# Optimization experiments

Hardware: AMD Instinct MI355X
Metric: run time of the kernel (lower is better)

## Reference

```python
import jax, jax.numpy as jnp
import numpy as np

B, T, D, NH, L = 8192, 100, 44, 64, 8  # batch, seq/ode steps, obs_dim, rnn hidden, latent


def setup_inputs() -> dict:
    key = jax.random.key(0)
    ks = jax.random.split(key, 12)
    s = 0.1
    return {
        "x": jax.random.normal(ks[0], (B, T, D), jnp.float32),
        "mask": jax.random.randint(ks[1], (B, T, D), 0, 2).astype(jnp.float32),
        "epsilon": jax.random.normal(ks[2], (B, L), jnp.float32),
        "Wi2h": jax.random.normal(ks[3], (D + NH, NH), jnp.float32) * s,
        "bi2h": jnp.zeros((NH,), jnp.float32),
        "Wh2o": jax.random.normal(ks[4], (NH, 2 * L), jnp.float32) * s,
        "bh2o": jnp.zeros((2 * L,), jnp.float32),
        "Wf1": jax.random.normal(ks[5], (L, NH), jnp.float32) * s,
        "bf1": jnp.zeros((NH,), jnp.float32),
        "Wf2": jax.random.normal(ks[6], (NH, NH), jnp.float32) * s,
        "bf2": jnp.zeros((NH,), jnp.float32),
        "Wf3": jax.random.normal(ks[7], (NH, L), jnp.float32) * s,
        "bf3": jnp.zeros((L,), jnp.float32),
        "Wd1": jax.random.normal(ks[8], (L, NH), jnp.float32) * s,
        "bd1": jnp.zeros((NH,), jnp.float32),
        "Wd2": jax.random.normal(ks[9], (NH, D), jnp.float32) * s,
        "bd2": jnp.zeros((D,), jnp.float32),
    }


def reference(x, mask, epsilon, Wi2h, bi2h, Wh2o, bh2o,
              Wf1, bf1, Wf2, bf2, Wf3, bf3, Wd1, bd1, Wd2, bd2):
    masked_x = x * mask  # [B,T,D]

    # --- reverse-time recognition RNN (scan over time, reversed) ---
    def rnn_step(h, obs):
        h = jnp.tanh(jnp.concatenate([obs, h], axis=1) @ Wi2h + bi2h)
        return h, None

    xs_rev = jnp.transpose(masked_x[:, ::-1, :], (1, 0, 2))  # [T,B,D]
    h0 = jnp.zeros((x.shape[0], Wi2h.shape[1]), x.dtype)
    h_final, _ = jax.lax.scan(rnn_step, h0, xs_rev)
    out = h_final @ Wh2o + bh2o  # [B,2L]
    qz0_mean, qz0_logvar = out[:, :L], out[:, L:]

    # reparameterized latent sample
    z0 = epsilon * jnp.exp(0.5 * qz0_logvar) + qz0_mean  # [B,L]

    # --- latent ODE dynamics, fixed-step RK4 over ts = linspace(0,1,100) ---
    def f(z):
        h1 = jax.nn.elu(z @ Wf1 + bf1)
        h2 = jax.nn.elu(h1 @ Wf2 + bf2)
        return h2 @ Wf3 + bf3

    dt = jnp.asarray(1.0 / (T - 1), x.dtype)

    def rk4_step(z, _):
        k1 = f(z)
        k2 = f(z + 0.5 * dt * k1)
        k3 = f(z + 0.5 * dt * k2)
        k4 = f(z + dt * k3)
        zn = z + (dt / 6.0) * (k1 + 2.0 * k2 + 2.0 * k3 + k4)
        return zn, zn

    _, zs = jax.lax.scan(rk4_step, z0, None, length=T - 1)  # [T-1,B,L]
    pred_z = jnp.transpose(jnp.concatenate([z0[None], zs], axis=0), (1, 0, 2))  # [B,T,L]

    # --- decoder ---
    pred_x = jax.nn.relu(pred_z @ Wd1 + bd1) @ Wd2 + bd2  # [B,T,D]

    # fill observed entries back in
    updated_x = jnp.where(masked_x != 0, masked_x, pred_x)

    # --- loss ---
    noise_logvar = 2.0 * jnp.log(jnp.asarray(0.3, x.dtype))
    log2pi = jnp.log(jnp.asarray(2.0 * np.pi, x.dtype))
    logpx = (-0.5 * (log2pi + noise_logvar +
                     (x - updated_x) ** 2 / jnp.exp(noise_logvar))).sum((-1, -2))  # [B]
    kl = (-0.5 * qz0_logvar + (jnp.exp(qz0_logvar) + qz0_mean ** 2) / 2.0 - 0.5).sum(-1)  # [B]
    loss = jnp.mean(-logpx + kl)
    return loss
```

## Files before the change

kernel.cpp:

```cpp
#include <hip/hip_runtime.h>
#include <stdint.h>


constexpr int B_ = 8192, T_ = 100, D_ = 44, NH_ = 64, L_ = 8;

typedef __bf16 bf16x8 __attribute__((ext_vector_type(8)));
typedef float f32x4 __attribute__((ext_vector_type(4)));
typedef uint32_t u32x4 __attribute__((ext_vector_type(4)));
typedef uint32_t u32x2 __attribute__((ext_vector_type(2)));

__device__ __forceinline__ float fexp2(float x) { return __builtin_amdgcn_exp2f(x); }
__device__ __forceinline__ float frcp(float x) { return __builtin_amdgcn_rcpf(x); }
__device__ __forceinline__ float fexp(float x) { return fexp2(x * 1.44269504088896341f); }
__device__ __forceinline__ float tanh_f(float x) {
  float e = fexp2(x * 2.88539008177792681f);
  return 1.0f - 2.0f * frcp(e + 1.0f);
}
__device__ __forceinline__ float elu_f(float x) { return x > 0.0f ? x : (fexp(x) - 1.0f); }
__device__ __forceinline__ uint32_t f2bs(float x) {
  return (uint32_t)__builtin_bit_cast(unsigned short, (__bf16)x);
}
__device__ __forceinline__ uint32_t pk(float lo, float hi) { return f2bs(lo) | (f2bs(hi) << 16); }
__device__ __forceinline__ uint32_t sh(uint32_t v, int s) { return (uint32_t)__shfl((int)v, s, 64); }
__device__ __forceinline__ f32x4 mfma16(bf16x8 a, bf16x8 b, f32x4 c) {
  return __builtin_amdgcn_mfma_f32_16x16x32_bf16(a, b, c, 0, 0, 0);
}
__device__ __forceinline__ bf16x8 pack8(float a, float b, float c, float d,
                                        float e, float f, float g, float h) {
  u32x4 u = {pk(a, b), pk(c, d), pk(e, f), pk(g, h)};
  return __builtin_bit_cast(bf16x8, u);
}
__device__ __forceinline__ float f4get(const float4& f, int i) {
  return i == 0 ? f.x : (i == 1 ? f.y : (i == 2 ? f.z : f.w));
}

__device__ __forceinline__ void repack_lds(uint32_t* tb, int c, int q,
                                           const f32x4* e, bf16x8* bh) {
#pragma unroll
  for (int tau = 0; tau < 4; ++tau) {
    u32x2 w = {pk(e[tau][0], e[tau][1]), pk(e[tau][2], e[tau][3])};
    *(u32x2*)(tb + 36 * c + 8 * tau + 2 * q) = w;
  }
#pragma unroll
  for (int ks = 0; ks < 2; ++ks) {
    u32x4 r = *(const u32x4*)(tb + 36 * c + 16 * ks + 4 * q);
    bh[ks] = __builtin_bit_cast(bf16x8, r);
  }
}

__device__ __forceinline__ bf16x8 build_bz(f32x4 z, int c, int q) {
  uint32_t p01 = pk(z[0], z[1]), p23 = pk(z[2], z[3]);
  u32x4 u = {sh(p01, c), sh(p23, c), sh(p01, c + 16), sh(p23, c + 16)};
  if (q == 1) u[0] = 0x3f80u;
  return __builtin_bit_cast(bf16x8, u);
}

__global__ __launch_bounds__(64) void fused_kernel(
    const float* __restrict__ x, const float* __restrict__ mask,
    const float* __restrict__ eps,
    const float* __restrict__ Wi2h, const float* __restrict__ bi2h,
    const float* __restrict__ Wh2o, const float* __restrict__ bh2o,
    const float* __restrict__ Wf1, const float* __restrict__ bf1,
    const float* __restrict__ Wf2, const float* __restrict__ bf2,
    const float* __restrict__ Wf3, const float* __restrict__ bf3,
    const float* __restrict__ Wd1, const float* __restrict__ bd1,
    const float* __restrict__ Wd2, const float* __restrict__ bd2,
    float* __restrict__ part) {
  const int lane = threadIdx.x;
  const int c = lane & 15, q = lane >> 4;
  const int r0 = blockIdx.x * 16;

  __shared__ uint32_t tbufA[576];
  __shared__ uint32_t tbufB[576];

  bf16x8 Ai[4][4];
#pragma unroll
  for (int tau = 0; tau < 4; ++tau)
#pragma unroll
    for (int ks = 0; ks < 4; ++ks) {
      bf16x8 f;
      const int m = 16 * tau + c;
#pragma unroll
      for (int i = 0; i < 8; ++i) {
        const int k = 32 * ks + 8 * q + i;
        float v = 0.0f;
        if (k < 64) v = Wi2h[(44 + k) * 64 + m];
        else if (k < 108) v = Wi2h[(k - 64) * 64 + m];
        else if (k == 108) v = bi2h[m];
        f[i] = (__bf16)v;
      }
      Ai[tau][ks] = f;
    }
  bf16x8 Ah2o[2];
#pragma unroll
  for (int ks = 0; ks < 2; ++ks) {
    bf16x8 f;
#pragma unroll
    for (int i = 0; i < 8; ++i) f[i] = (__bf16)Wh2o[(32 * ks + 8 * q + i) * 16 + c];
    Ah2o[ks] = f;
  }
  f32x4 bo;
#pragma unroll
  for (int r = 0; r < 4; ++r) bo[r] = bh2o[4 * q + r];

  const float* xrowbase = x + (size_t)(r0 + c) * T_ * D_;
  const float* mrowbase = mask + (size_t)(r0 + c) * T_ * D_;

  auto load_obs = [&](int t, float4& a0, float4& a1, float4& b0, float4& b1,
                      float4& ma0, float4& ma1, float4& mb0, float4& mb1) {
    const float4* xr = (const float4*)(xrowbase + (size_t)t * D_);
    const float4* mr = (const float4*)(mrowbase + (size_t)t * D_);
    a0 = xr[2 * q]; a1 = xr[2 * q + 1]; ma0 = mr[2 * q]; ma1 = mr[2 * q + 1];
    float4 zz = {0.f, 0.f, 0.f, 0.f};
    b0 = zz; b1 = zz; mb0 = zz; mb1 = zz;
    if (q == 0) { b0 = xr[8]; b1 = xr[9]; mb0 = mr[8]; mb1 = mr[9]; }
    else if (q == 1) { b0 = xr[10]; mb0 = mr[10]; }
  };

  f32x4 hc[4] = {};
  float4 a0, a1, b0, b1, ma0, ma1, mb0, mb1;
  load_obs(T_ - 1, a0, a1, b0, b1, ma0, ma1, mb0, mb1);

#pragma unroll 1
  for (int s = 0; s < T_; ++s) {
    const int t = T_ - 1 - s;
    float4 ca0 = a0, ca1 = a1, cb0 = b0, cb1 = b1;
    float4 cm0 = ma0, cm1 = ma1, cn0 = mb0, cn1 = mb1;
    if (t > 0) load_obs(t - 1, a0, a1, b0, b1, ma0, ma1, mb0, mb1);

    bf16x8 bh[2];
    repack_lds(tbufA, c, q, hc, bh);
    bf16x8 o2 = pack8(ca0.x * cm0.x, ca0.y * cm0.y, ca0.z * cm0.z, ca0.w * cm0.w,
                      ca1.x * cm1.x, ca1.y * cm1.y, ca1.z * cm1.z, ca1.w * cm1.w);
    const float e44 = (q == 1) ? 1.0f : cb1.x * cn1.x;
    bf16x8 o3 = pack8(cb0.x * cn0.x, cb0.y * cn0.y, cb0.z * cn0.z, cb0.w * cn0.w,
                      e44, cb1.y * cn1.y, cb1.z * cn1.z, cb1.w * cn1.w);
#pragma unroll
    for (int tau = 0; tau < 4; ++tau) {
      f32x4 zero = {0.f, 0.f, 0.f, 0.f};
      f32x4 acc = mfma16(Ai[tau][0], bh[0], zero);
      acc = mfma16(Ai[tau][1], bh[1], acc);
      acc = mfma16(Ai[tau][2], o2, acc);
      acc = mfma16(Ai[tau][3], o3, acc);
#pragma unroll
      for (int r = 0; r < 4; ++r) hc[tau][r] = tanh_f(acc[r]);
    }
  }

  bf16x8 bhF[2];
  repack_lds(tbufA, c, q, hc, bhF);
  f32x4 o = mfma16(Ah2o[1], bhF[1], mfma16(Ah2o[0], bhF[0], bo));

  float lv[4];
#pragma unroll
  for (int r = 0; r < 4; ++r)
    lv[r] = __int_as_float(__shfl(__float_as_int(o[r]), lane + 32, 64));

  float klt = 0.0f;
  f32x4 z = {};
  if (q < 2) {
    const float4 ev = *(const float4*)(eps + (size_t)(r0 + c) * 8 + 4 * q);
#pragma unroll
    for (int r = 0; r < 4; ++r) {
      const float m = o[r];
      z[r] = f4get(ev, r) * fexp(0.5f * lv[r]) + m;
      klt += -0.5f * lv[r] + (fexp(lv[r]) + m * m) * 0.5f - 0.5f;
    }
  }
  klt += __shfl_xor(klt, 1);  klt += __shfl_xor(klt, 2);
  klt += __shfl_xor(klt, 4);  klt += __shfl_xor(klt, 8);
  klt += __shfl_xor(klt, 16); klt += __shfl_xor(klt, 32);

  __builtin_amdgcn_sched_barrier(0);

  bf16x8 A1[4], A2[4][2], A3[2], Ad1[4], Ad2[3][2];
#pragma unroll
  for (int tau = 0; tau < 4; ++tau) {
    bf16x8 f1, fd;
#pragma unroll
    for (int i = 0; i < 8; ++i) {
      const int k = 8 * q + i;
      f1[i] = (__bf16)(k < 8 ? Wf1[k * 64 + 16 * tau + c] : (k == 8 ? bf1[16 * tau + c] : 0.0f));
      fd[i] = (__bf16)(k < 8 ? Wd1[k * 64 + 16 * tau + c] : (k == 8 ? bd1[16 * tau + c] : 0.0f));
    }
    A1[tau] = f1; Ad1[tau] = fd;
#pragma unroll
    for (int ks = 0; ks < 2; ++ks) {
      bf16x8 g;
#pragma unroll
      for (int i = 0; i < 8; ++i) g[i] = (__bf16)Wf2[(32 * ks + 8 * q + i) * 64 + 16 * tau + c];
      A2[tau][ks] = g;
    }
  }
#pragma unroll
  for (int ks = 0; ks < 2; ++ks) {
    bf16x8 f;
#pragma unroll
    for (int i = 0; i < 8; ++i)
      f[i] = (__bf16)((c < 8) ? Wf3[(32 * ks + 8 * q + i) * 8 + c] : 0.0f);
    A3[ks] = f;
  }
#pragma unroll
  for (int tau = 0; tau < 3; ++tau)
#pragma unroll
    for (int ks = 0; ks < 2; ++ks) {
      bf16x8 f;
      const int m = 16 * tau + c;
#pragma unroll
      for (int i = 0; i < 8; ++i)
        f[i] = (__bf16)((m < 44) ? Wd2[(32 * ks + 8 * q + i) * 44 + m] : 0.0f);
      Ad2[tau][ks] = f;
    }
  f32x4 b2_[4], b3_, bd2_[3];
#pragma unroll
  for (int tau = 0; tau < 4; ++tau)
#pragma unroll
    for (int r = 0; r < 4; ++r) b2_[tau][r] = bf2[16 * tau + 4 * q + r];
#pragma unroll
  for (int r = 0; r < 4; ++r) b3_[r] = (q < 2) ? bf3[4 * q + r] : 0.0f;
#pragma unroll
  for (int tau = 0; tau < 3; ++tau)
#pragma unroll
    for (int r = 0; r < 4; ++r) {
      const int d = 16 * tau + 4 * q + r;
      bd2_[tau][r] = (d < 44) ? bd2[d] : 0.0f;
    }

  auto feval = [&](bf16x8 bz) -> f32x4 {
    f32x4 h[4];
#pragma unroll
    for (int tau = 0; tau < 4; ++tau) {
      f32x4 zero = {0.f, 0.f, 0.f, 0.f};
      h[tau] = mfma16(A1[tau], bz, zero);
#pragma unroll
      for (int r = 0; r < 4; ++r) h[tau][r] = elu_f(h[tau][r]);
    }
    bf16x8 bh[2];
    repack_lds(tbufA, c, q, h, bh);
    f32x4 g[4];
#pragma unroll
    for (int tau = 0; tau < 4; ++tau) {
      g[tau] = mfma16(A2[tau][1], bh[1], mfma16(A2[tau][0], bh[0], b2_[tau]));
#pragma unroll
      for (int r = 0; r < 4; ++r) g[tau][r] = elu_f(g[tau][r]);
    }
    bf16x8 bg[2];
    repack_lds(tbufA, c, q, g, bg);
    return mfma16(A3[1], bg[1], mfma16(A3[0], bg[0], b3_));
  };

  auto load_xm = [&](int t, float4* xv, float4* mv) {
#pragma unroll
    for (int tau = 0; tau < 3; ++tau) {
      const int d0 = 16 * tau + 4 * q;
      if (d0 < 44) {
        const size_t off = (size_t)(r0 + c) * T_ * D_ + (size_t)t * D_ + d0;
        xv[tau] = *(const float4*)(x + off);
        mv[tau] = *(const float4*)(mask + off);
      }
    }
  };

  const float dt = 1.0f / (float)(T_ - 1);
  const float hdt = 0.5f * dt;
  float qacc = 0.0f;

  float4 xc[3], mc[3], xn[3], mn[3];
  load_xm(0, xc, mc);

#pragma unroll 1
  for (int t = 0; t < T_; ++t) {
    if (t < T_ - 1) load_xm(t + 1, xn, mn);

    bf16x8 bz = build_bz(z, c, q);

    f32x4 hd[4];
#pragma unroll
    for (int tau = 0; tau < 4; ++tau) {
      f32x4 zero = {0.f, 0.f, 0.f, 0.f};
      hd[tau] = mfma16(Ad1[tau], bz, zero);
#pragma unroll
      for (int r = 0; r < 4; ++r) hd[tau][r] = fmaxf(hd[tau][r], 0.0f);
    }
    bf16x8 bhd[2];
    repack_lds(tbufB, c, q, hd, bhd);
#pragma unroll
    for (int tau = 0; tau < 3; ++tau) {
      f32x4 p = mfma16(Ad2[tau][1], bhd[1], mfma16(Ad2[tau][0], bhd[0], bd2_[tau]));
      if (16 * tau + 4 * q < 44) {
#pragma unroll
        for (int r = 0; r < 4; ++r) {
          const float xa = f4get(xc[tau], r), ma = f4get(mc[tau], r);
          const float mx = xa * ma;
          const float upd = (mx != 0.0f) ? mx : p[r];
          const float df = xa - upd;
          qacc += df * df;
        }
      }
    }

    if (t < T_ - 1) {
      f32x4 k1 = feval(bz);
      f32x4 zt;
#pragma unroll
      for (int r = 0; r < 4; ++r) zt[r] = z[r] + hdt * k1[r];
      f32x4 k2 = feval(build_bz(zt, c, q));
#pragma unroll
      for (int r = 0; r < 4; ++r) zt[r] = z[r] + hdt * k2[r];
      f32x4 k3 = feval(build_bz(zt, c, q));
#pragma unroll
      for (int r = 0; r < 4; ++r) zt[r] = z[r] + dt * k3[r];
      f32x4 k4 = feval(build_bz(zt, c, q));
#pragma unroll
      for (int r = 0; r < 4; ++r)
        z[r] += (dt / 6.0f) * (k1[r] + 2.0f * (k2[r] + k3[r]) + k4[r]);
#pragma unroll
      for (int tau = 0; tau < 3; ++tau) { xc[tau] = xn[tau]; mc[tau] = mn[tau]; }
    }
  }

  float tot = qacc * (0.5f / 0.09f);
  tot += __shfl_xor(tot, 1);  tot += __shfl_xor(tot, 2);
  tot += __shfl_xor(tot, 4);  tot += __shfl_xor(tot, 8);
  tot += __shfl_xor(tot, 16); tot += __shfl_xor(tot, 32);
  if (lane == 0) part[blockIdx.x] = tot + klt;
}

__global__ __launch_bounds__(512) void reduce_kernel(const float* __restrict__ part,
                                                     float* __restrict__ out) {
  __shared__ float s[8];
  const int tid = threadIdx.x;
  float v = part[tid];
  v += __shfl_xor(v, 1);  v += __shfl_xor(v, 2);
  v += __shfl_xor(v, 4);  v += __shfl_xor(v, 8);
  v += __shfl_xor(v, 16); v += __shfl_xor(v, 32);
  if ((tid & 63) == 0) s[tid >> 6] = v;
  __syncthreads();
  if (tid == 0) {
    float acc = 0.0f;
#pragma unroll
    for (int i = 0; i < 8; ++i) acc += s[i];
    const float c0 = 0.28503427112126353f;
    out[0] = acc * (1.0f / (float)B_) - (float)(T_ * D_) * c0;
  }
}

extern "C" void kernel_launch(void* const* d_in, const int* in_sizes, int n_in,
                              void* d_out, int out_size, void* d_ws, size_t ws_size,
                              hipStream_t stream) {
  const float* x    = (const float*)d_in[0];
  const float* mask = (const float*)d_in[1];
  const float* eps  = (const float*)d_in[2];
  const float* Wi2h = (const float*)d_in[3];
  const float* bi2h = (const float*)d_in[4];
  const float* Wh2o = (const float*)d_in[5];
  const float* bh2o = (const float*)d_in[6];
  const float* Wf1  = (const float*)d_in[7];
  const float* bf1  = (const float*)d_in[8];
  const float* Wf2  = (const float*)d_in[9];
  const float* bf2  = (const float*)d_in[10];
  const float* Wf3  = (const float*)d_in[11];
  const float* bf3  = (const float*)d_in[12];
  const float* Wd1  = (const float*)d_in[13];
  const float* bd1  = (const float*)d_in[14];
  const float* Wd2  = (const float*)d_in[15];
  const float* bd2  = (const float*)d_in[16];

  float* loss = (float*)d_out;
  float* part = (float*)d_ws;

  fused_kernel<<<dim3(B_ / 16), dim3(64), 0, stream>>>(
      x, mask, eps, Wi2h, bi2h, Wh2o, bh2o, Wf1, bf1, Wf2, bf2, Wf3, bf3,
      Wd1, bd1, Wd2, bd2, part);
  reduce_kernel<<<dim3(1), dim3(512), 0, stream>>>(part, loss);
}
```

Baseline: 826.9 us.

## Split hidden-unit tiles across four waves per block with LDS exchange

Each 16-row batch tile now runs on a 256-thread block in which every wave owns one 16-wide slice of the 64 hidden units. The four tau tiles that one wave used to compute serially are spread across waves, and hidden states are exchanged through double-buffered LDS with a workgroup barrier at each layer. The goal is to cut the serial MFMA and transcendental chain per timestep and to hold fewer weight registers per wave. The cost is several barriers per RNN and RK4 step, plus more waves per block, which could shift occupancy.

Result: faster. 757.2 us (-8.4%).

```diff
diff --git a/kernel.cpp b/kernel.cpp
--- a/kernel.cpp
+++ b/kernel.cpp
@@ -34,16 +34,20 @@
   return i == 0 ? f.x : (i == 1 ? f.y : (i == 2 ? f.z : f.w));
 }
 
-__device__ __forceinline__ void repack_lds(uint32_t* tb, int c, int q,
-                                           const f32x4* e, bf16x8* bh) {
-#pragma unroll
-  for (int tau = 0; tau < 4; ++tau) {
-    u32x2 w = {pk(e[tau][0], e[tau][1]), pk(e[tau][2], e[tau][3])};
-    *(u32x2*)(tb + 36 * c + 8 * tau + 2 * q) = w;
-  }
-#pragma unroll
-  for (int ks = 0; ks < 2; ++ks) {
-    u32x4 r = *(const u32x4*)(tb + 36 * c + 16 * ks + 4 * q);
+__device__ __forceinline__ void xbar() {
+  asm volatile("s_waitcnt lgkmcnt(0)" ::: "memory");
+  __builtin_amdgcn_s_barrier();
+  asm volatile("" ::: "memory");
+}
+
+__device__ __forceinline__ void ex_write(uint32_t* ex, int c, int q, int w, f32x4 e) {
+  u32x2 v = {pk(e[0], e[1]), pk(e[2], e[3])};
+  *(u32x2*)(ex + 36 * c + 8 * w + 2 * q) = v;
+}
+__device__ __forceinline__ void ex_read(const uint32_t* ex, int c, int q, bf16x8* bh) {
+#pragma unroll
+  for (int ks = 0; ks < 2; ++ks) {
+    u32x4 r = *(const u32x4*)(ex + 36 * c + 16 * ks + 4 * q);
     bh[ks] = __builtin_bit_cast(bf16x8, r);
   }
 }
@@ -55,7 +59,7 @@
   return __builtin_bit_cast(bf16x8, u);
 }
 
-__global__ __launch_bounds__(64) void fused_kernel(
+__global__ __launch_bounds__(256) void fused_kernel(
     const float* __restrict__ x, const float* __restrict__ mask,
     const float* __restrict__ eps,
     const float* __restrict__ Wi2h, const float* __restrict__ bi2h,
@@ -66,31 +70,33 @@
     const float* __restrict__ Wd1, const float* __restrict__ bd1,
     const float* __restrict__ Wd2, const float* __restrict__ bd2,
     float* __restrict__ part) {
-  const int lane = threadIdx.x;
+  const int tid = threadIdx.x;
+  const int w = tid >> 6;
+  const int lane = tid & 63;
   const int c = lane & 15, q = lane >> 4;
   const int r0 = blockIdx.x * 16;
 
-  __shared__ uint32_t tbufA[576];
-  __shared__ uint32_t tbufB[576];
-
-  bf16x8 Ai[4][4];
-#pragma unroll
-  for (int tau = 0; tau < 4; ++tau)
-#pragma unroll
-    for (int ks = 0; ks < 4; ++ks) {
-      bf16x8 f;
-      const int m = 16 * tau + c;
-#pragma unroll
-      for (int i = 0; i < 8; ++i) {
-        const int k = 32 * ks + 8 * q + i;
-        float v = 0.0f;
-        if (k < 64) v = Wi2h[(44 + k) * 64 + m];
-        else if (k < 108) v = Wi2h[(k - 64) * 64 + m];
-        else if (k == 108) v = bi2h[m];
-        f[i] = (__bf16)v;
-      }
-      Ai[tau][ks] = f;
-    }
+  __shared__ __align__(16) uint32_t exA[576];
+  __shared__ __align__(16) uint32_t exB[576];
+  __shared__ __align__(16) uint32_t exC[576];
+  __shared__ float redbuf[4];
+
+  bf16x8 Ai[4];
+#pragma unroll
+  for (int ks = 0; ks < 4; ++ks) {
+    bf16x8 f;
+    const int m = 16 * w + c;
+#pragma unroll
+    for (int i = 0; i < 8; ++i) {
+      const int k = 32 * ks + 8 * q + i;
+      float v = 0.0f;
+      if (k < 64) v = Wi2h[(44 + k) * 64 + m];
+      else if (k < 108) v = Wi2h[(k - 64) * 64 + m];
+      else if (k == 108) v = bi2h[m];
+      f[i] = (__bf16)v;
+    }
+    Ai[ks] = f;
+  }
   bf16x8 Ah2o[2];
 #pragma unroll
   for (int ks = 0; ks < 2; ++ks) {
@@ -117,38 +123,43 @@
     else if (q == 1) { b0 = xr[10]; mb0 = mr[10]; }
   };
 
-  f32x4 hc[4] = {};
+  f32x4 hc = {0.f, 0.f, 0.f, 0.f};
   float4 a0, a1, b0, b1, ma0, ma1, mb0, mb1;
   load_obs(T_ - 1, a0, a1, b0, b1, ma0, ma1, mb0, mb1);
 
 #pragma unroll 1
   for (int s = 0; s < T_; ++s) {
+    uint32_t* ex = (s & 1) ? exB : exA;
+    ex_write(ex, c, q, w, hc);
+
     const int t = T_ - 1 - s;
     float4 ca0 = a0, ca1 = a1, cb0 = b0, cb1 = b1;
     float4 cm0 = ma0, cm1 = ma1, cn0 = mb0, cn1 = mb1;
     if (t > 0) load_obs(t - 1, a0, a1, b0, b1, ma0, ma1, mb0, mb1);
 
-    bf16x8 bh[2];
-    repack_lds(tbufA, c, q, hc, bh);
     bf16x8 o2 = pack8(ca0.x * cm0.x, ca0.y * cm0.y, ca0.z * cm0.z, ca0.w * cm0.w,
                       ca1.x * cm1.x, ca1.y * cm1.y, ca1.z * cm1.z, ca1.w * cm1.w);
     const float e44 = (q == 1) ? 1.0f : cb1.x * cn1.x;
     bf16x8 o3 = pack8(cb0.x * cn0.x, cb0.y * cn0.y, cb0.z * cn0.z, cb0.w * cn0.w,
                       e44, cb1.y * cn1.y, cb1.z * cn1.z, cb1.w * cn1.w);
-#pragma unroll
-    for (int tau = 0; tau < 4; ++tau) {
-      f32x4 zero = {0.f, 0.f, 0.f, 0.f};
-      f32x4 acc = mfma16(Ai[tau][0], bh[0], zero);
-      acc = mfma16(Ai[tau][1], bh[1], acc);
-      acc = mfma16(Ai[tau][2], o2, acc);
-      acc = mfma16(Ai[tau][3], o3, acc);
-#pragma unroll
-      for (int r = 0; r < 4; ++r) hc[tau][r] = tanh_f(acc[r]);
-    }
-  }
-
+
+    xbar();
+    bf16x8 bh[2];
+    ex_read(ex, c, q, bh);
+
+    f32x4 zero = {0.f, 0.f, 0.f, 0.f};
+    f32x4 acc = mfma16(Ai[0], bh[0], zero);
+    acc = mfma16(Ai[1], bh[1], acc);
+    acc = mfma16(Ai[2], o2, acc);
+    acc = mfma16(Ai[3], o3, acc);
+#pragma unroll
+    for (int r = 0; r < 4; ++r) hc[r] = tanh_f(acc[r]);
+  }
+
+  ex_write(exA, c, q, w, hc);
+  xbar();
   bf16x8 bhF[2];
-  repack_lds(tbufA, c, q, hc, bhF);
+  ex_read(exA, c, q, bhF);
   f32x4 o = mfma16(Ah2o[1], bhF[1], mfma16(Ah2o[0], bhF[0], bo));
 
   float lv[4];
@@ -173,24 +184,23 @@
 
   __builtin_amdgcn_sched_barrier(0);
 
-  bf16x8 A1[4], A2[4][2], A3[2], Ad1[4], Ad2[3][2];
-#pragma unroll
-  for (int tau = 0; tau < 4; ++tau) {
+  bf16x8 A1, A2[2], A3[2], Ad1, Ad2[2];
+  {
     bf16x8 f1, fd;
 #pragma unroll
     for (int i = 0; i < 8; ++i) {
       const int k = 8 * q + i;
-      f1[i] = (__bf16)(k < 8 ? Wf1[k * 64 + 16 * tau + c] : (k == 8 ? bf1[16 * tau + c] : 0.0f));
-      fd[i] = (__bf16)(k < 8 ? Wd1[k * 64 + 16 * tau + c] : (k == 8 ? bd1[16 * tau + c] : 0.0f));
-    }
-    A1[tau] = f1; Ad1[tau] = fd;
-#pragma unroll
-    for (int ks = 0; ks < 2; ++ks) {
-      bf16x8 g;
-#pragma unroll
-      for (int i = 0; i < 8; ++i) g[i] = (__bf16)Wf2[(32 * ks + 8 * q + i) * 64 + 16 * tau + c];
-      A2[tau][ks] = g;
-    }
+      f1[i] = (__bf16)(k < 8 ? Wf1[k * 64 + 16 * w + c] : (k == 8 ? bf1[16 * w + c] : 0.0f));
+      fd[i] = (__bf16)(k < 8 ? Wd1[k * 64 + 16 * w + c] : (k == 8 ? bd1[16 * w + c] : 0.0f));
+    }
+    A1 = f1; Ad1 = fd;
+  }
+#pragma unroll
+  for (int ks = 0; ks < 2; ++ks) {
+    bf16x8 g;
+#pragma unroll
+    for (int i = 0; i < 8; ++i) g[i] = (__bf16)Wf2[(32 * ks + 8 * q + i) * 64 + 16 * w + c];
+    A2[ks] = g;
   }
 #pragma unroll
   for (int ks = 0; ks < 2; ++ks) {
@@ -201,63 +211,50 @@
     A3[ks] = f;
   }
 #pragma unroll
-  for (int tau = 0; tau < 3; ++tau)
-#pragma unroll
-    for (int ks = 0; ks < 2; ++ks) {
-      bf16x8 f;
-      const int m = 16 * tau + c;
-#pragma unroll
-      for (int i = 0; i < 8; ++i)
-        f[i] = (__bf16)((m < 44) ? Wd2[(32 * ks + 8 * q + i) * 44 + m] : 0.0f);
-      Ad2[tau][ks] = f;
-    }
-  f32x4 b2_[4], b3_, bd2_[3];
-#pragma unroll
-  for (int tau = 0; tau < 4; ++tau)
-#pragma unroll
-    for (int r = 0; r < 4; ++r) b2_[tau][r] = bf2[16 * tau + 4 * q + r];
+  for (int ks = 0; ks < 2; ++ks) {
+    bf16x8 f;
+    const int m = 16 * w + c;
+#pragma unroll
+    for (int i = 0; i < 8; ++i)
+      f[i] = (__bf16)((m < 44) ? Wd2[(32 * ks + 8 * q + i) * 44 + m] : 0.0f);
+    Ad2[ks] = f;
+  }
+  f32x4 b2_, b3_, bd2_;
+#pragma unroll
+  for (int r = 0; r < 4; ++r) b2_[r] = bf2[16 * w + 4 * q + r];
 #pragma unroll
   for (int r = 0; r < 4; ++r) b3_[r] = (q < 2) ? bf3[4 * q + r] : 0.0f;
 #pragma unroll
-  for (int tau = 0; tau < 3; ++tau)
-#pragma unroll
-    for (int r = 0; r < 4; ++r) {
-      const int d = 16 * tau + 4 * q + r;
-      bd2_[tau][r] = (d < 44) ? bd2[d] : 0.0f;
-    }
+  for (int r = 0; r < 4; ++r) {
+    const int d = 16 * w + 4 * q + r;
+    bd2_[r] = (d < 44) ? bd2[d] : 0.0f;
+  }
 
   auto feval = [&](bf16x8 bz) -> f32x4 {
-    f32x4 h[4];
-#pragma unroll
-    for (int tau = 0; tau < 4; ++tau) {
-      f32x4 zero = {0.f, 0.f, 0.f, 0.f};
-      h[tau] = mfma16(A1[tau], bz, zero);
-#pragma unroll
-      for (int r = 0; r < 4; ++r) h[tau][r] = elu_f(h[tau][r]);
-    }
+    f32x4 zero = {0.f, 0.f, 0.f, 0.f};
+    f32x4 h = mfma16(A1, bz, zero);
+#pragma unroll
+    for (int r = 0; r < 4; ++r) h[r] = elu_f(h[r]);
+    ex_write(exA, c, q, w, h);
+    xbar();
     bf16x8 bh[2];
-    repack_lds(tbufA, c, q, h, bh);
-    f32x4 g[4];
-#pragma unroll
-    for (int tau = 0; tau < 4; ++tau) {
-      g[tau] = mfma16(A2[tau][1], bh[1], mfma16(A2[tau][0], bh[0], b2_[tau]));
-#pragma unroll
-      for (int r = 0; r < 4; ++r) g[tau][r] = elu_f(g[tau][r]);
-    }
+    ex_read(exA, c, q, bh);
+    f32x4 g = mfma16(A2[1], bh[1], mfma16(A2[0], bh[0], b2_));
+#pragma unroll
+    for (int r = 0; r < 4; ++r) g[r] = elu_f(g[r]);
+    ex_write(exB, c, q, w, g);
+    xbar();
     bf16x8 bg[2];
-    repack_lds(tbufA, c, q, g, bg);
+    ex_read(exB, c, q, bg);
     return mfma16(A3[1], bg[1], mfma16(A3[0], bg[0], b3_));
   };
 
-  auto load_xm = [&](int t, float4* xv, float4* mv) {
-#pragma unroll
-    for (int tau = 0; tau < 3; ++tau) {
-      const int d0 = 16 * tau + 4 * q;
-      if (d0 < 44) {
-        const size_t off = (size_t)(r0 + c) * T_ * D_ + (size_t)t * D_ + d0;
-        xv[tau] = *(const float4*)(x + off);
-        mv[tau] = *(const float4*)(mask + off);
-      }
+  auto load_xm = [&](int t, float4& xv, float4& mv) {
+    const int d0 = 16 * w + 4 * q;
+    if (w < 3 && d0 < 44) {
+      const size_t off = (size_t)(r0 + c) * T_ * D_ + (size_t)t * D_ + d0;
+      xv = *(const float4*)(x + off);
+      mv = *(const float4*)(mask + off);
     }
   };
 
@@ -265,7 +262,7 @@
   const float hdt = 0.5f * dt;
   float qacc = 0.0f;
 
-  float4 xc[3], mc[3], xn[3], mn[3];
+  float4 xc = {0.f, 0.f, 0.f, 0.f}, mc = xc, xn = xc, mn = xc;
   load_xm(0, xc, mc);
 
 #pragma unroll 1
@@ -274,23 +271,20 @@
 
     bf16x8 bz = build_bz(z, c, q);
 
-    f32x4 hd[4];
-#pragma unroll
-    for (int tau = 0; tau < 4; ++tau) {
-      f32x4 zero = {0.f, 0.f, 0.f, 0.f};
-      hd[tau] = mfma16(Ad1[tau], bz, zero);
-#pragma unroll
-      for (int r = 0; r < 4; ++r) hd[tau][r] = fmaxf(hd[tau][r], 0.0f);
-    }
-    bf16x8 bhd[2];
-    repack_lds(tbufB, c, q, hd, bhd);
-#pragma unroll
-    for (int tau = 0; tau < 3; ++tau) {
-      f32x4 p = mfma16(Ad2[tau][1], bhd[1], mfma16(Ad2[tau][0], bhd[0], bd2_[tau]));
-      if (16 * tau + 4 * q < 44) {
+    f32x4 zero = {0.f, 0.f, 0.f, 0.f};
+    f32x4 hd = mfma16(Ad1, bz, zero);
+#pragma unroll
+    for (int r = 0; r < 4; ++r) hd[r] = fmaxf(hd[r], 0.0f);
+    ex_write(exC, c, q, w, hd);
+    xbar();
+    if (w < 3) {
+      bf16x8 bhd[2];
+      ex_read(exC, c, q, bhd);
+      f32x4 p = mfma16(Ad2[1], bhd[1], mfma16(Ad2[0], bhd[0], bd2_));
+      if (16 * w + 4 * q < 44) {
 #pragma unroll
         for (int r = 0; r < 4; ++r) {
-          const float xa = f4get(xc[tau], r), ma = f4get(mc[tau], r);
+          const float xa = f4get(xc, r), ma = f4get(mc, r);
           const float mx = xa * ma;
           const float upd = (mx != 0.0f) ? mx : p[r];
           const float df = xa - upd;
@@ -314,8 +308,7 @@
 #pragma unroll
       for (int r = 0; r < 4; ++r)
         z[r] += (dt / 6.0f) * (k1[r] + 2.0f * (k2[r] + k3[r]) + k4[r]);
-#pragma unroll
-      for (int tau = 0; tau < 3; ++tau) { xc[tau] = xn[tau]; mc[tau] = mn[tau]; }
+      xc = xn; mc = mn;
     }
   }
 
@@ -323,7 +316,10 @@
   tot += __shfl_xor(tot, 1);  tot += __shfl_xor(tot, 2);
   tot += __shfl_xor(tot, 4);  tot += __shfl_xor(tot, 8);
   tot += __shfl_xor(tot, 16); tot += __shfl_xor(tot, 32);
-  if (lane == 0) part[blockIdx.x] = tot + klt;
+  if (lane == 0) redbuf[w] = tot;
+  xbar();
+  if (tid == 0)
+    part[blockIdx.x] = redbuf[0] + redbuf[1] + redbuf[2] + redbuf[3] + klt;
 }
 
 __global__ __launch_bounds__(512) void reduce_kernel(const float* __restrict__ part,
@@ -369,7 +365,7 @@
   float* loss = (float*)d_out;
   float* part = (float*)d_ws;
 
-  fused_kernel<<<dim3(B_ / 16), dim3(64), 0, stream>>>(
+  fused_kernel<<<dim3(B_ / 16), dim3(256), 0, stream>>>(
       x, mask, eps, Wi2h, bi2h, Wh2o, bh2o, Wf1, bf1, Wf2, bf2, Wf3, bf3,
       Wd1, bd1, Wd2, bd2, part);
   reduce_kernel<<<dim3(1), dim3(512), 0, stream>>>(part, loss);
```

## Switch to 16x16x16 MFMA so accumulator layout feeds next B operand without LDS

Applied to the files above, without the earlier changes.

Replaces the 16x16x32 bf16 MFMA with the 16x16x16 variant, whose C/D fragment layout (4 rows per lane group) matches the B operand layout. This lets each layer's output be packed directly in registers as the next layer's input, removing the LDS write/read repacks and the shuffles in build_bz. It doubles the MFMA instruction count for the same K and splits the RNN accumulation into two independent chains to shorten dependency latency.

New measurement: 698.0 us. 15.6% less time.

```diff
diff --git a/kernel.cpp b/kernel.cpp
--- a/kernel.cpp
+++ b/kernel.cpp
@@ -4,10 +4,26 @@
 
 constexpr int B_ = 8192, T_ = 100, D_ = 44, NH_ = 64, L_ = 8;
 
-typedef __bf16 bf16x8 __attribute__((ext_vector_type(8)));
 typedef float f32x4 __attribute__((ext_vector_type(4)));
-typedef uint32_t u32x4 __attribute__((ext_vector_type(4)));
 typedef uint32_t u32x2 __attribute__((ext_vector_type(2)));
+
+#if __has_builtin(__builtin_amdgcn_mfma_f32_16x16x16bf16_1k)
+typedef short frag16 __attribute__((ext_vector_type(4)));
+#define MFMA16(a, b, c) __builtin_amdgcn_mfma_f32_16x16x16bf16_1k(a, b, c, 0, 0, 0)
+#define USE_F16 0
+#elif __has_builtin(__builtin_amdgcn_mfma_f32_16x16x16_bf16_1k)
+typedef short frag16 __attribute__((ext_vector_type(4)));
+#define MFMA16(a, b, c) __builtin_amdgcn_mfma_f32_16x16x16_bf16_1k(a, b, c, 0, 0, 0)
+#define USE_F16 0
+#elif __has_builtin(__builtin_amdgcn_mfma_f32_16x16x16_bf16)
+typedef __bf16 frag16 __attribute__((ext_vector_type(4)));
+#define MFMA16(a, b, c) __builtin_amdgcn_mfma_f32_16x16x16_bf16(a, b, c, 0, 0, 0)
+#define USE_F16 0
+#else
+typedef _Float16 frag16 __attribute__((ext_vector_type(4)));
+#define MFMA16(a, b, c) __builtin_amdgcn_mfma_f32_16x16x16f16(a, b, c, 0, 0, 0)
+#define USE_F16 1
+#endif
 
 __device__ __forceinline__ float fexp2(float x) { return __builtin_amdgcn_exp2f(x); }
 __device__ __forceinline__ float frcp(float x) { return __builtin_amdgcn_rcpf(x); }
@@ -17,42 +33,25 @@
   return 1.0f - 2.0f * frcp(e + 1.0f);
 }
 __device__ __forceinline__ float elu_f(float x) { return x > 0.0f ? x : (fexp(x) - 1.0f); }
-__device__ __forceinline__ uint32_t f2bs(float x) {
-  return (uint32_t)__builtin_bit_cast(unsigned short, (__bf16)x);
-}
-__device__ __forceinline__ uint32_t pk(float lo, float hi) { return f2bs(lo) | (f2bs(hi) << 16); }
-__device__ __forceinline__ uint32_t sh(uint32_t v, int s) { return (uint32_t)__shfl((int)v, s, 64); }
-__device__ __forceinline__ f32x4 mfma16(bf16x8 a, bf16x8 b, f32x4 c) {
-  return __builtin_amdgcn_mfma_f32_16x16x32_bf16(a, b, c, 0, 0, 0);
-}
-__device__ __forceinline__ bf16x8 pack8(float a, float b, float c, float d,
-                                        float e, float f, float g, float h) {
-  u32x4 u = {pk(a, b), pk(c, d), pk(e, f), pk(g, h)};
-  return __builtin_bit_cast(bf16x8, u);
+
+__device__ __forceinline__ uint32_t EW(float v) {
+#if USE_F16
+  return (uint32_t)__builtin_bit_cast(unsigned short, (_Float16)v);
+#else
+  return (uint32_t)__builtin_bit_cast(unsigned short, (__bf16)v);
+#endif
+}
+__device__ __forceinline__ uint32_t PK2(float lo, float hi) { return EW(lo) | (EW(hi) << 16); }
+__device__ __forceinline__ frag16 fr4(float a, float b, float c, float d) {
+  u32x2 u = {PK2(a, b), PK2(c, d)};
+  return __builtin_bit_cast(frag16, u);
+}
+__device__ __forceinline__ frag16 frpk(f32x4 v) {
+  u32x2 u = {PK2(v[0], v[1]), PK2(v[2], v[3])};
+  return __builtin_bit_cast(frag16, u);
 }
 __device__ __forceinline__ float f4get(const float4& f, int i) {
   return i == 0 ? f.x : (i == 1 ? f.y : (i == 2 ? f.z : f.w));
-}
-
-__device__ __forceinline__ void repack_lds(uint32_t* tb, int c, int q,
-                                           const f32x4* e, bf16x8* bh) {
-#pragma unroll
-  for (int tau = 0; tau < 4; ++tau) {
-    u32x2 w = {pk(e[tau][0], e[tau][1]), pk(e[tau][2], e[tau][3])};
-    *(u32x2*)(tb + 36 * c + 8 * tau + 2 * q) = w;
-  }
-#pragma unroll
-  for (int ks = 0; ks < 2; ++ks) {
-    u32x4 r = *(const u32x4*)(tb + 36 * c + 16 * ks + 4 * q);
-    bh[ks] = __builtin_bit_cast(bf16x8, r);
-  }
-}
-
-__device__ __forceinline__ bf16x8 build_bz(f32x4 z, int c, int q) {
-  uint32_t p01 = pk(z[0], z[1]), p23 = pk(z[2], z[3]);
-  u32x4 u = {sh(p01, c), sh(p23, c), sh(p01, c + 16), sh(p23, c + 16)};
-  if (q == 1) u[0] = 0x3f80u;
-  return __builtin_bit_cast(bf16x8, u);
 }
 
 __global__ __launch_bounds__(64) void fused_kernel(
@@ -69,35 +68,34 @@
   const int lane = threadIdx.x;
   const int c = lane & 15, q = lane >> 4;
   const int r0 = blockIdx.x * 16;
-
-  __shared__ uint32_t tbufA[576];
-  __shared__ uint32_t tbufB[576];
-
-  bf16x8 Ai[4][4];
+  const f32x4 fzero = {0.f, 0.f, 0.f, 0.f};
+  const frag16 fgbias = fr4(1.0f, 0.f, 0.f, 0.f);
+
+  frag16 Ai[4][7];
 #pragma unroll
   for (int tau = 0; tau < 4; ++tau)
 #pragma unroll
-    for (int ks = 0; ks < 4; ++ks) {
-      bf16x8 f;
+    for (int kc = 0; kc < 7; ++kc) {
       const int m = 16 * tau + c;
-#pragma unroll
-      for (int i = 0; i < 8; ++i) {
-        const int k = 32 * ks + 8 * q + i;
+      float wv[4];
+#pragma unroll
+      for (int i = 0; i < 4; ++i) {
+        const int k = 16 * kc + 4 * q + i;
         float v = 0.0f;
         if (k < 64) v = Wi2h[(44 + k) * 64 + m];
         else if (k < 108) v = Wi2h[(k - 64) * 64 + m];
         else if (k == 108) v = bi2h[m];
-        f[i] = (__bf16)v;
+        wv[i] = v;
       }
-      Ai[tau][ks] = f;
-    }
-  bf16x8 Ah2o[2];
-#pragma unroll
-  for (int ks = 0; ks < 2; ++ks) {
-    bf16x8 f;
-#pragma unroll
-    for (int i = 0; i < 8; ++i) f[i] = (__bf16)Wh2o[(32 * ks + 8 * q + i) * 16 + c];
-    Ah2o[ks] = f;
+      Ai[tau][kc] = fr4(wv[0], wv[1], wv[2], wv[3]);
+    }
+  frag16 Ah2o[4];
+#pragma unroll
+  for (int kc = 0; kc < 4; ++kc) {
+    float wv[4];
+#pragma unroll
+    for (int i = 0; i < 4; ++i) wv[i] = Wh2o[(16 * kc + 4 * q + i) * 16 + c];
+    Ah2o[kc] = fr4(wv[0], wv[1], wv[2], wv[3]);
   }
   f32x4 bo;
 #pragma unroll
@@ -106,50 +104,70 @@
   const float* xrowbase = x + (size_t)(r0 + c) * T_ * D_;
   const float* mrowbase = mask + (size_t)(r0 + c) * T_ * D_;
 
-  auto load_obs = [&](int t, float4& a0, float4& a1, float4& b0, float4& b1,
-                      float4& ma0, float4& ma1, float4& mb0, float4& mb1) {
-    const float4* xr = (const float4*)(xrowbase + (size_t)t * D_);
-    const float4* mr = (const float4*)(mrowbase + (size_t)t * D_);
-    a0 = xr[2 * q]; a1 = xr[2 * q + 1]; ma0 = mr[2 * q]; ma1 = mr[2 * q + 1];
+  auto load_obs = [&](int t, float4* xv, float4* mv) {
+    const float* xp = xrowbase + (size_t)t * D_;
+    const float* mp = mrowbase + (size_t)t * D_;
+    xv[0] = *(const float4*)(xp + 4 * q);
+    mv[0] = *(const float4*)(mp + 4 * q);
+    xv[1] = *(const float4*)(xp + 16 + 4 * q);
+    mv[1] = *(const float4*)(mp + 16 + 4 * q);
     float4 zz = {0.f, 0.f, 0.f, 0.f};
-    b0 = zz; b1 = zz; mb0 = zz; mb1 = zz;
-    if (q == 0) { b0 = xr[8]; b1 = xr[9]; mb0 = mr[8]; mb1 = mr[9]; }
-    else if (q == 1) { b0 = xr[10]; mb0 = mr[10]; }
+    xv[2] = zz; mv[2] = zz;
+    if (q < 3) {
+      xv[2] = *(const float4*)(xp + 32 + 4 * q);
+      mv[2] = *(const float4*)(mp + 32 + 4 * q);
+    }
   };
 
   f32x4 hc[4] = {};
-  float4 a0, a1, b0, b1, ma0, ma1, mb0, mb1;
-  load_obs(T_ - 1, a0, a1, b0, b1, ma0, ma1, mb0, mb1);
+  float4 xo[3], mo[3];
+  load_obs(T_ - 1, xo, mo);
 
 #pragma unroll 1
   for (int s = 0; s < T_; ++s) {
     const int t = T_ - 1 - s;
-    float4 ca0 = a0, ca1 = a1, cb0 = b0, cb1 = b1;
-    float4 cm0 = ma0, cm1 = ma1, cn0 = mb0, cn1 = mb1;
-    if (t > 0) load_obs(t - 1, a0, a1, b0, b1, ma0, ma1, mb0, mb1);
-
-    bf16x8 bh[2];
-    repack_lds(tbufA, c, q, hc, bh);
-    bf16x8 o2 = pack8(ca0.x * cm0.x, ca0.y * cm0.y, ca0.z * cm0.z, ca0.w * cm0.w,
-                      ca1.x * cm1.x, ca1.y * cm1.y, ca1.z * cm1.z, ca1.w * cm1.w);
-    const float e44 = (q == 1) ? 1.0f : cb1.x * cn1.x;
-    bf16x8 o3 = pack8(cb0.x * cn0.x, cb0.y * cn0.y, cb0.z * cn0.z, cb0.w * cn0.w,
-                      e44, cb1.y * cn1.y, cb1.z * cn1.z, cb1.w * cn1.w);
+    float4 cx[3], cm[3];
+#pragma unroll
+    for (int j = 0; j < 3; ++j) { cx[j] = xo[j]; cm[j] = mo[j]; }
+    if (t > 0) load_obs(t - 1, xo, mo);
+
+    frag16 ob[3];
+#pragma unroll
+    for (int j = 0; j < 2; ++j) {
+      u32x2 u = {PK2(cx[j].x * cm[j].x, cx[j].y * cm[j].y),
+                 PK2(cx[j].z * cm[j].z, cx[j].w * cm[j].w)};
+      ob[j] = __builtin_bit_cast(frag16, u);
+    }
+    {
+      u32x2 u = {PK2(cx[2].x * cm[2].x, cx[2].y * cm[2].y),
+                 PK2(cx[2].z * cm[2].z, cx[2].w * cm[2].w)};
+      ob[2] = (q < 3) ? __builtin_bit_cast(frag16, u) : fgbias;
+    }
+
+    frag16 bh[4];
+#pragma unroll
+    for (int tau = 0; tau < 4; ++tau) bh[tau] = frpk(hc[tau]);
+
 #pragma unroll
     for (int tau = 0; tau < 4; ++tau) {
-      f32x4 zero = {0.f, 0.f, 0.f, 0.f};
-      f32x4 acc = mfma16(Ai[tau][0], bh[0], zero);
-      acc = mfma16(Ai[tau][1], bh[1], acc);
-      acc = mfma16(Ai[tau][2], o2, acc);
-      acc = mfma16(Ai[tau][3], o3, acc);
-#pragma unroll
-      for (int r = 0; r < 4; ++r) hc[tau][r] = tanh_f(acc[r]);
-    }
-  }
-
-  bf16x8 bhF[2];
-  repack_lds(tbufA, c, q, hc, bhF);
-  f32x4 o = mfma16(Ah2o[1], bhF[1], mfma16(Ah2o[0], bhF[0], bo));
+      f32x4 aA = MFMA16(Ai[tau][0], bh[0], fzero);
+      aA = MFMA16(Ai[tau][1], bh[1], aA);
+      aA = MFMA16(Ai[tau][2], bh[2], aA);
+      aA = MFMA16(Ai[tau][3], bh[3], aA);
+      f32x4 aB = MFMA16(Ai[tau][4], ob[0], fzero);
+      aB = MFMA16(Ai[tau][5], ob[1], aB);
+      aB = MFMA16(Ai[tau][6], ob[2], aB);
+#pragma unroll
+      for (int r = 0; r < 4; ++r) hc[tau][r] = tanh_f(aA[r] + aB[r]);
+    }
+  }
+
+  frag16 bhF[4];
+#pragma unroll
+  for (int tau = 0; tau < 4; ++tau) bhF[tau] = frpk(hc[tau]);
+  f32x4 o = bo;
+#pragma unroll
+  for (int kc = 0; kc < 4; ++kc) o = MFMA16(Ah2o[kc], bhF[kc], o);
 
   float lv[4];
 #pragma unroll
@@ -173,43 +191,46 @@
 
   __builtin_amdgcn_sched_barrier(0);
 
-  bf16x8 A1[4], A2[4][2], A3[2], Ad1[4], Ad2[3][2];
+  frag16 A1[4], A2[4][4], A3[4], Ad1[4], Ad2[3][4];
 #pragma unroll
   for (int tau = 0; tau < 4; ++tau) {
-    bf16x8 f1, fd;
-#pragma unroll
-    for (int i = 0; i < 8; ++i) {
-      const int k = 8 * q + i;
-      f1[i] = (__bf16)(k < 8 ? Wf1[k * 64 + 16 * tau + c] : (k == 8 ? bf1[16 * tau + c] : 0.0f));
-      fd[i] = (__bf16)(k < 8 ? Wd1[k * 64 + 16 * tau + c] : (k == 8 ? bd1[16 * tau + c] : 0.0f));
-    }
-    A1[tau] = f1; Ad1[tau] = fd;
-#pragma unroll
-    for (int ks = 0; ks < 2; ++ks) {
-      bf16x8 g;
-#pragma unroll
-      for (int i = 0; i < 8; ++i) g[i] = (__bf16)Wf2[(32 * ks + 8 * q + i) * 64 + 16 * tau + c];
-      A2[tau][ks] = g;
-    }
-  }
-#pragma unroll
-  for (int ks = 0; ks < 2; ++ks) {
-    bf16x8 f;
-#pragma unroll
-    for (int i = 0; i < 8; ++i)
-      f[i] = (__bf16)((c < 8) ? Wf3[(32 * ks + 8 * q + i) * 8 + c] : 0.0f);
-    A3[ks] = f;
+    float w1[4], wd[4];
+#pragma unroll
+    for (int i = 0; i < 4; ++i) {
+      const int k = 4 * q + i;
+      w1[i] = k < 8 ? Wf1[k * 64 + 16 * tau + c] : (k == 8 ? bf1[16 * tau + c] : 0.0f);
+      wd[i] = k < 8 ? Wd1[k * 64 + 16 * tau + c] : (k == 8 ? bd1[16 * tau + c] : 0.0f);
+    }
+    A1[tau] = fr4(w1[0], w1[1], w1[2], w1[3]);
+    Ad1[tau] = fr4(wd[0], wd[1], wd[2], wd[3]);
+  }
+#pragma unroll
+  for (int tau = 0; tau < 4; ++tau)
+#pragma unroll
+    for (int kc = 0; kc < 4; ++kc) {
+      float wv[4];
+#pragma unroll
+      for (int i = 0; i < 4; ++i) wv[i] = Wf2[(16 * kc + 4 * q + i) * 64 + 16 * tau + c];
+      A2[tau][kc] = fr4(wv[0], wv[1], wv[2], wv[3]);
+    }
+#pragma unroll
+  for (int kc = 0; kc < 4; ++kc) {
+    float wv[4];
+#pragma unroll
+    for (int i = 0; i < 4; ++i)
+      wv[i] = (c < 8) ? Wf3[(16 * kc + 4 * q + i) * 8 + c] : 0.0f;
+    A3[kc] = fr4(wv[0], wv[1], wv[2], wv[3]);
   }
 #pragma unroll
   for (int tau = 0; tau < 3; ++tau)
 #pragma unroll
-    for (int ks = 0; ks < 2; ++ks) {
-      bf16x8 f;
+    for (int kc = 0; kc < 4; ++kc) {
       const int m = 16 * tau + c;
-#pragma unroll
-      for (int i = 0; i < 8; ++i)
-        f[i] = (__bf16)((m < 44) ? Wd2[(32 * ks + 8 * q + i) * 44 + m] : 0.0f);
-      Ad2[tau][ks] = f;
+      float wv[4];
+#pragma unroll
+      for (int i = 0; i < 4; ++i)
+        wv[i] = (m < 44) ? Wd2[(16 * kc + 4 * q + i) * 44 + m] : 0.0f;
+      Ad2[tau][kc] = fr4(wv[0], wv[1], wv[2], wv[3]);
     }
   f32x4 b2_[4], b3_, bd2_[3];
 #pragma unroll
@@ -226,27 +247,36 @@
       bd2_[tau][r] = (d < 44) ? bd2[d] : 0.0f;
     }
 
-  auto feval = [&](bf16x8 bz) -> f32x4 {
-    f32x4 h[4];
+  auto build_bz = [&](f32x4 zv) -> frag16 {
+    u32x2 u = {PK2(zv[0], zv[1]), PK2(zv[2], zv[3])};
+    if (q == 2) { u[0] = EW(1.0f); u[1] = 0u; }
+    else if (q == 3) { u[0] = 0u; u[1] = 0u; }
+    return __builtin_bit_cast(frag16, u);
+  };
+
+  auto feval = [&](frag16 bz) -> f32x4 {
+    frag16 bh[4];
 #pragma unroll
     for (int tau = 0; tau < 4; ++tau) {
-      f32x4 zero = {0.f, 0.f, 0.f, 0.f};
-      h[tau] = mfma16(A1[tau], bz, zero);
-#pragma unroll
-      for (int r = 0; r < 4; ++r) h[tau][r] = elu_f(h[tau][r]);
-    }
-    bf16x8 bh[2];
-    repack_lds(tbufA, c, q, h, bh);
-    f32x4 g[4];
+      f32x4 h = MFMA16(A1[tau], bz, fzero);
+#pragma unroll
+      for (int r = 0; r < 4; ++r) h[r] = elu_f(h[r]);
+      bh[tau] = frpk(h);
+    }
+    frag16 bg[4];
 #pragma unroll
     for (int tau = 0; tau < 4; ++tau) {
-      g[tau] = mfma16(A2[tau][1], bh[1], mfma16(A2[tau][0], bh[0], b2_[tau]));
-#pragma unroll
-      for (int r = 0; r < 4; ++r) g[tau][r] = elu_f(g[tau][r]);
-    }
-    bf16x8 bg[2];
-    repack_lds(tbufA, c, q, g, bg);
-    return mfma16(A3[1], bg[1], mfma16(A3[0], bg[0], b3_));
+      f32x4 g = b2_[tau];
+#pragma unroll
+      for (int kc = 0; kc < 4; ++kc) g = MFMA16(A2[tau][kc], bh[kc], g);
+#pragma unroll
+      for (int r = 0; r < 4; ++r) g[r] = elu_f(g[r]);
+      bg[tau] = frpk(g);
+    }
+    f32x4 rr = b3_;
+#pragma unroll
+    for (int kc = 0; kc < 4; ++kc) rr = MFMA16(A3[kc], bg[kc], rr);
+    return rr;
   };
 
   auto load_xm = [&](int t, float4* xv, float4* mv) {
@@ -272,21 +302,21 @@
   for (int t = 0; t < T_; ++t) {
     if (t < T_ - 1) load_xm(t + 1, xn, mn);
 
-    bf16x8 bz = build_bz(z, c, q);
-
-    f32x4 hd[4];
+    frag16 bz = build_bz(z);
+
+    frag16 bhd[4];
 #pragma unroll
     for (int tau = 0; tau < 4; ++tau) {
-      f32x4 zero = {0.f, 0.f, 0.f, 0.f};
-      hd[tau] = mfma16(Ad1[tau], bz, zero);
-#pragma unroll
-      for (int r = 0; r < 4; ++r) hd[tau][r] = fmaxf(hd[tau][r], 0.0f);
-    }
-    bf16x8 bhd[2];
-    repack_lds(tbufB, c, q, hd, bhd);
+      f32x4 hd = MFMA16(Ad1[tau], bz, fzero);
+#pragma unroll
+      for (int r = 0; r < 4; ++r) hd[r] = fmaxf(hd[r], 0.0f);
+      bhd[tau] = frpk(hd);
+    }
 #pragma unroll
     for (int tau = 0; tau < 3; ++tau) {
-      f32x4 p = mfma16(Ad2[tau][1], bhd[1], mfma16(Ad2[tau][0], bhd[0], bd2_[tau]));
+      f32x4 p = bd2_[tau];
+#pragma unroll
+      for (int kc = 0; kc < 4; ++kc) p = MFMA16(Ad2[tau][kc], bhd[kc], p);
       if (16 * tau + 4 * q < 44) {
 #pragma unroll
         for (int r = 0; r < 4; ++r) {
@@ -304,13 +334,13 @@
       f32x4 zt;
 #pragma unroll
       for (int r = 0; r < 4; ++r) zt[r] = z[r] + hdt * k1[r];
-      f32x4 k2 = feval(build_bz(zt, c, q));
+      f32x4 k2 = feval(build_bz(zt));
 #pragma unroll
       for (int r = 0; r < 4; ++r) zt[r] = z[r] + hdt * k2[r];
-      f32x4 k3 = feval(build_bz(zt, c, q));
+      f32x4 k3 = feval(build_bz(zt));
 #pragma unroll
       for (int r = 0; r < 4; ++r) zt[r] = z[r] + dt * k3[r];
-      f32x4 k4 = feval(build_bz(zt, c, q));
+      f32x4 k4 = feval(build_bz(zt));
 #pragma unroll
       for (int r = 0; r < 4; ++r)
         z[r] += (dt / 6.0f) * (k1[r] + 2.0f * (k2[r] + k3[r]) + k4[r]);
```
